# Kernel optimization log

Hardware: AMD Instinct MI355X
Metric: run time of the kernel (lower is better)

The kernel has to match this reference:

```python
import jax, jax.numpy as jnp
import numpy as np
import math

N_NODES = 100000
N_EDGES = 1600000
IN_DIM = 32
OUT_DIM = 32

def setup_inputs() -> dict:
    key = jax.random.key(0)
    k1, k2, k3, k4 = jax.random.split(key, 4)
    X = jax.random.normal(k1, (N_NODES, IN_DIM), dtype=jnp.float32)
    src_idx = jax.random.randint(k2, (N_EDGES,), 0, N_NODES, dtype=jnp.int64)
    dst_idx = jax.random.randint(k3, (N_EDGES,), 0, N_NODES, dtype=jnp.int64)
    # weights init: uniform(-stdv, stdv), stdv = 1/sqrt(output_dim)
    stdv = 1.0 / math.sqrt(OUT_DIM)
    W = jax.random.uniform(k4, (IN_DIM, OUT_DIM), dtype=jnp.float32,
                           minval=-stdv, maxval=stdv)
    return {"X": X, "W": W, "src_idx": src_idx, "dst_idx": dst_idx}

def reference(X, W, src_idx, dst_idx):
    # GIN sum-aggregation SpMM: agg[i] = sum_{j in N(i)} X[j]
    agg = jax.ops.segment_sum(X[src_idx], dst_idx, num_segments=N_NODES)
    # dense GEMM: X_prime = agg @ W
    return agg @ W
```

## Files before the change

kernel.cpp:

```cpp
#include <hip/hip_runtime.h>

#define N_DIM 32
#define NPB 64
#define NB_FINE_MAX 2048
#define CAPFINE 1280
#define CAPB 16
#define CEPB 4096
#define NSEG_PAD 512
#define FT 512
#define GROWS 512

__device__ __forceinline__ unsigned f2bf_rne(float f) {
    unsigned u = __float_as_uint(f);
    return (u + 0x7FFFu + ((u >> 16) & 1u)) >> 16;
}
__device__ __forceinline__ float bf2f(unsigned h) {
    return __uint_as_float(h << 16);
}

__global__ __launch_bounds__(FT) void k_fused(const float* __restrict__ X,
                                              const float* __restrict__ W,
                                              unsigned* __restrict__ Y,
                                              const int* __restrict__ src,
                                              const int* __restrict__ dst,
                                              int* __restrict__ cnt2,
                                              int* __restrict__ pairs2,
                                              int n_nodes, int n_edges,
                                              int nbins, int nblk_g) {
    __shared__ float Wlds[N_DIM * N_DIM];
    __shared__ int h[NB_FINE_MAX];
    const int t = threadIdx.x;

    if (blockIdx.x < nblk_g) {
        for (int i = t; i < N_DIM * N_DIM; i += FT) Wlds[i] = W[i];
        __syncthreads();
        const int r = blockIdx.x * GROWS + t;
        if (r >= n_nodes) return;

        float x[N_DIM];
        const float4* xr = (const float4*)(X + (size_t)r * N_DIM);
#pragma unroll
        for (int i = 0; i < N_DIM / 4; ++i) {
            float4 v = xr[i];
            x[4 * i + 0] = v.x; x[4 * i + 1] = v.y;
            x[4 * i + 2] = v.z; x[4 * i + 3] = v.w;
        }
        float acc[N_DIM];
#pragma unroll
        for (int c = 0; c < N_DIM; ++c) acc[c] = 0.0f;
#pragma unroll
        for (int k = 0; k < N_DIM; ++k) {
            const float xk = x[k];
#pragma unroll
            for (int c = 0; c < N_DIM; ++c)
                acc[c] = fmaf(xk, Wlds[k * N_DIM + c], acc[c]);
        }
        unsigned yp[16];
#pragma unroll
        for (int q = 0; q < 16; ++q)
            yp[q] = f2bf_rne(acc[2 * q]) | (f2bf_rne(acc[2 * q + 1]) << 16);
        uint4* yr = (uint4*)(Y + (size_t)r * 16);
#pragma unroll
        for (int i = 0; i < 4; ++i)
            yr[i] = make_uint4(yp[4 * i], yp[4 * i + 1],
                               yp[4 * i + 2], yp[4 * i + 3]);
    } else {
        for (int i = t; i < nbins; i += FT) h[i] = 0;
        __syncthreads();
        const int seg = blockIdx.x - nblk_g;
        const int start = seg * CEPB;
        int* __restrict__ myseg = pairs2 + (size_t)seg * nbins * CAPB;

        int vw[CEPB / FT], cw[CEPB / FT], rw[CEPB / FT];
#pragma unroll
        for (int k = 0; k < CEPB / FT; ++k) {
            int e = start + t + k * FT;
            if (e < n_edges) {
                int d = dst[e];
                cw[k] = d >> 6;
                vw[k] = src[e] | ((d & 63) << 17);
                rw[k] = atomicAdd(&h[cw[k]], 1);
            } else {
                cw[k] = -1;
            }
        }
#pragma unroll
        for (int k = 0; k < CEPB / FT; ++k)
            if (cw[k] >= 0 && rw[k] < CAPB)
                myseg[(size_t)cw[k] * CAPB + rw[k]] = vw[k];
        __syncthreads();
        for (int i = t; i < nbins; i += FT)
            cnt2[(size_t)seg * nbins + i] = min(h[i], CAPB);
    }
}

__device__ __forceinline__ void addv(float* acc, uint4 v) {
    acc[0] += bf2f(v.x & 0xFFFFu); acc[1] += bf2f(v.x >> 16);
    acc[2] += bf2f(v.y & 0xFFFFu); acc[3] += bf2f(v.y >> 16);
    acc[4] += bf2f(v.z & 0xFFFFu); acc[5] += bf2f(v.z >> 16);
    acc[6] += bf2f(v.w & 0xFFFFu); acc[7] += bf2f(v.w >> 16);
}

__global__ __launch_bounds__(256) void k_agg(const uint4* __restrict__ Y4,
                                             const int* __restrict__ cnt2,
                                             const int* __restrict__ pairs2,
                                             float* __restrict__ out,
                                             int n_nodes, int nbins, int nseg) {
    __shared__ int qbuf[CAPFINE];
    __shared__ int sbin[CAPFINE];
    __shared__ int scnt[NSEG_PAD];
    __shared__ int soff[NSEG_PAD];
    __shared__ int slen;
    __shared__ int cnt[NPB];
    __shared__ int cst[NPB];
    __shared__ int excl[NPB];

    const int t = threadIdx.x;
    const int b = blockIdx.x;

    for (int i = t; i < NSEG_PAD; i += 256)
        scnt[i] = (i < nseg) ? cnt2[(size_t)i * nbins + b] : 0;
    __syncthreads();

    if (t < 64) {
        int run = 0;
#pragma unroll
        for (int ch = 0; ch < NSEG_PAD / 64; ++ch) {
            int a = scnt[ch * 64 + t];
            int x = a;
#pragma unroll
            for (int o = 1; o < 64; o <<= 1) {
                int u = __shfl_up(x, o, 64);
                if (t >= o) x += u;
            }
            soff[ch * 64 + t] = run + x - a;
            run += __shfl(x, 63, 64);
        }
        if (t == 0) slen = run;
    }
    if (t < NPB) cnt[t] = 0;
    __syncthreads();
    const int len = min(slen, CAPFINE);

    for (int s = t; s < nseg; s += 256) {
        int c = scnt[s];
        int o = soff[s];
        const int* cell = pairs2 + ((size_t)s * nbins + b) * CAPB;
        for (int j = 0; j < c; ++j) {
            int idx = o + j;
            if (idx < CAPFINE) qbuf[idx] = cell[j];
        }
    }
    __syncthreads();

    int pv[CAPFINE / 256], rv[CAPFINE / 256];
#pragma unroll
    for (int k = 0; k < CAPFINE / 256; ++k) {
        int i = t + k * 256;
        if (i < len) {
            int p = qbuf[i];
            pv[k] = p;
            rv[k] = atomicAdd(&cnt[(p >> 17) & 63], 1);
        } else {
            pv[k] = -1;
        }
    }
    __syncthreads();
    if (t < 64) {
        int c0 = cnt[t];
        int c = c0;
#pragma unroll
        for (int off = 1; off < 64; off <<= 1) {
            int u = __shfl_up(c, off, 64);
            if (t >= off) c += u;
        }
        cst[t] = c;
        excl[t] = c - c0;
    }
    __syncthreads();
#pragma unroll
    for (int k = 0; k < CAPFINE / 256; ++k) {
        if (pv[k] >= 0) {
            int p = pv[k];
            sbin[excl[(p >> 17) & 63] + rv[k]] = p & 0x1FFFF;
        }
    }
    __syncthreads();

    const int g = t >> 2;
    const int l = t & 3;
    float acc[8];
#pragma unroll
    for (int i = 0; i < 8; ++i) acc[i] = 0.0f;

    const int s1 = cst[g];
    const int s0 = s1 - cnt[g];
    for (int e = s0; e < s1; e += 4) {
        const int m = s1 - e;
        int i0 = sbin[e];
        int i1 = sbin[e + ((m > 1) ? 1 : 0)];
        int i2 = sbin[e + ((m > 2) ? 2 : 0)];
        int i3 = sbin[e + ((m > 3) ? 3 : 0)];
        uint4 v0 = Y4[(size_t)i0 * 4 + l];
        uint4 v1 = Y4[(size_t)i1 * 4 + l];
        uint4 v2 = Y4[(size_t)i2 * 4 + l];
        uint4 v3 = Y4[(size_t)i3 * 4 + l];
        addv(acc, v0);
        if (m > 1) addv(acc, v1);
        if (m > 2) addv(acc, v2);
        if (m > 3) addv(acc, v3);
    }

    const int node = b * NPB + g;
    if (node < n_nodes) {
        ((float4*)out)[(size_t)node * 8 + 2 * l] =
            make_float4(acc[0], acc[1], acc[2], acc[3]);
        ((float4*)out)[(size_t)node * 8 + 2 * l + 1] =
            make_float4(acc[4], acc[5], acc[6], acc[7]);
    }
}

extern "C" void kernel_launch(void* const* d_in, const int* in_sizes, int n_in,
                              void* d_out, int out_size, void* d_ws, size_t ws_size,
                              hipStream_t stream) {
    const float* X   = (const float*)d_in[0];
    const float* W   = (const float*)d_in[1];
    const int*   src = (const int*)d_in[2];
    const int*   dst = (const int*)d_in[3];
    float* out = (float*)d_out;

    const int n_nodes = in_sizes[0] / N_DIM;
    const int n_edges = in_sizes[2];
    const int nbins = (n_nodes + NPB - 1) / NPB;
    const int nseg  = (n_edges + CEPB - 1) / CEPB;

    unsigned* Y  = (unsigned*)d_ws;
    int* cnt2    = (int*)(Y + (size_t)n_nodes * 16);
    int* pairs2  = cnt2 + (size_t)nseg * nbins;

    const int nblk_g = (n_nodes + GROWS - 1) / GROWS;

    k_fused<<<nblk_g + nseg, FT, 0, stream>>>(X, W, Y, src, dst, cnt2, pairs2,
                                              n_nodes, n_edges, nbins, nblk_g);
    k_agg<<<nbins, 256, 0, stream>>>((const uint4*)Y, cnt2, pairs2, out,
                                     n_nodes, nbins, nseg);
}
```

Before: 130.9 us.

## Transpose edge bucket layout to bin-major for coalesced aggregation reads

Stores the per-segment, per-bin edge buckets bin-major instead of segment-major, so each aggregation block's data is contiguous. The aggregation kernel then streams its region with coalesced 16-byte loads and filters each slot by its per-segment count. This replaces many small dependent per-cell loops with wide loads. In exchange, every padded slot is read even when mostly empty, and the scatter writes in the binning kernel become widely strided.

```diff
diff --git a/kernel.cpp b/kernel.cpp
--- a/kernel.cpp
+++ b/kernel.cpp
@@ -26,7 +26,7 @@
                                               int* __restrict__ cnt2,
                                               int* __restrict__ pairs2,
                                               int n_nodes, int n_edges,
-                                              int nbins, int nblk_g) {
+                                              int nbins, int nseg, int nblk_g) {
     __shared__ float Wlds[N_DIM * N_DIM];
     __shared__ int h[NB_FINE_MAX];
     const int t = threadIdx.x;
@@ -69,7 +69,8 @@
         __syncthreads();
         const int seg = blockIdx.x - nblk_g;
         const int start = seg * CEPB;
-        int* __restrict__ myseg = pairs2 + (size_t)seg * nbins * CAPB;
+        int* __restrict__ mybase = pairs2 + (size_t)seg * CAPB;
+        const size_t binstride = (size_t)nseg * CAPB;
 
         int vw[CEPB / FT], cw[CEPB / FT], rw[CEPB / FT];
 #pragma unroll
@@ -87,7 +88,7 @@
 #pragma unroll
         for (int k = 0; k < CEPB / FT; ++k)
             if (cw[k] >= 0 && rw[k] < CAPB)
-                myseg[(size_t)cw[k] * CAPB + rw[k]] = vw[k];
+                mybase[(size_t)cw[k] * binstride + rw[k]] = vw[k];
         __syncthreads();
         for (int i = t; i < nbins; i += FT)
             cnt2[(size_t)seg * nbins + i] = min(h[i], CAPB);
@@ -142,13 +143,24 @@
     __syncthreads();
     const int len = min(slen, CAPFINE);
 
-    for (int s = t; s < nseg; s += 256) {
-        int c = scnt[s];
-        int o = soff[s];
-        const int* cell = pairs2 + ((size_t)s * nbins + b) * CAPB;
-        for (int j = 0; j < c; ++j) {
-            int idx = o + j;
-            if (idx < CAPFINE) qbuf[idx] = cell[j];
+    {
+        const uint4* reg4 = (const uint4*)(pairs2 + (size_t)b * nseg * CAPB);
+        const int tot4 = nseg * CAPB / 4;
+        for (int i4 = t; i4 < tot4; i4 += 256) {
+            uint4 v = reg4[i4];
+            const int s = i4 / (CAPB / 4);
+            const int j0 = (i4 % (CAPB / 4)) * 4;
+            const int c = scnt[s];
+            const int o = soff[s];
+            unsigned pv4[4] = {v.x, v.y, v.z, v.w};
+#pragma unroll
+            for (int j = 0; j < 4; ++j) {
+                const int jj = j0 + j;
+                if (jj < c) {
+                    int idx = o + jj;
+                    if (idx < CAPFINE) qbuf[idx] = (int)pv4[j];
+                }
+            }
         }
     }
     __syncthreads();
@@ -241,7 +253,7 @@
     const int nblk_g = (n_nodes + GROWS - 1) / GROWS;
 
     k_fused<<<nblk_g + nseg, FT, 0, stream>>>(X, W, Y, src, dst, cnt2, pairs2,
-                                              n_nodes, n_edges, nbins, nblk_g);
+                                              n_nodes, n_edges, nbins, nseg, nblk_g);
     k_agg<<<nbins, 256, 0, stream>>>((const uint4*)Y, cnt2, pairs2, out,
                                      n_nodes, nbins, nseg);
 }
```

Result: faster. 127.1 us (-2.9%).
